# Performance work log

Measured on AMD Instinct MI355X. Metric: run time of the kernel, lower is better.

## Reference

```python
import math
import jax, jax.numpy as jnp
import numpy as np

BLOCK_K = 128  # key/value block size; S_k % BLOCK_K == 0 so no padding/mask needed


def setup_inputs() -> dict:
    key = jax.random.key(0)
    kq, kk, kv = jax.random.split(key, 3)
    B, S, H, Hkv, D = 1, 4096, 16, 8, 128
    return {
        "query": jax.random.normal(kq, (B, S, H, D), dtype=jnp.float32),
        "key": jax.random.normal(kk, (B, S, Hkv, D), dtype=jnp.float32),
        "value": jax.random.normal(kv, (B, S, Hkv, D), dtype=jnp.float32),
    }


def _ring_attention(query, key, value, block_k=BLOCK_K):
    # query: [B, Sq, H, D]; key/value: [B, Sk, Hkv, D]
    scale = 1.0 / math.sqrt(query.shape[-1])
    reps = query.shape[2] // key.shape[2]
    if reps > 1:  # GQA: repeat kv heads to match query heads
        key = jnp.repeat(key, reps, axis=2)
        value = jnp.repeat(value, reps, axis=2)
    q = jnp.transpose(query, (0, 2, 1, 3))   # [B, H, Sq, D]
    k = jnp.transpose(key, (0, 2, 1, 3))     # [B, H, Sk, D]
    v = jnp.transpose(value, (0, 2, 1, 3))
    B, H, Sq, D = q.shape
    Sk = k.shape[2]
    nk = Sk // block_k
    # split keys/values into blocks, block axis leading for scan
    kb = k.reshape(B, H, nk, block_k, D).transpose(2, 0, 1, 3, 4)
    vb = v.reshape(B, H, nk, block_k, D).transpose(2, 0, 1, 3, 4)
    m0 = jnp.full((B, H, Sq), -jnp.inf, dtype=jnp.float32)
    l0 = jnp.zeros((B, H, Sq), dtype=jnp.float32)
    o0 = jnp.zeros((B, H, Sq, D), dtype=jnp.float32)

    def step(carry, kv_blk):
        m, l, o = carry
        k_blk, v_blk = kv_blk
        scores = jnp.einsum('bhqd,bhkd->bhqk', q, k_blk) * scale
        m_new = jnp.maximum(m, jnp.max(scores, axis=-1))
        alpha = jnp.exp(m - m_new)                     # rescale factor (0 on first step)
        p = jnp.exp(scores - m_new[..., None])
        l = l * alpha + jnp.sum(p, axis=-1)
        o = o * alpha[..., None] + jnp.einsum('bhqk,bhkd->bhqd', p, v_blk)
        return (m_new, l, o), None

    (m, l, o), _ = jax.lax.scan(step, (m0, l0, o0), (kb, vb))
    out = o / l[..., None]
    return jnp.transpose(out, (0, 2, 1, 3))  # [B, Sq, H, D]


def reference(query, key, value):
    return _ring_attention(query, key, value)
```

## Files before the change

kernel.cpp:

```cpp
#include <hip/hip_runtime.h>
#include <math.h>


namespace {
constexpr int NH  = 16;
constexpr int NKV = 8;
constexpr int DH  = 128;
constexpr int SK  = 4096;
constexpr int TQ  = 128;
constexpr int NT  = 256;

constexpr int BKM   = 32;
constexpr int NKTM  = SK / BKM;
constexpr int TILEM = BKM * DH;
constexpr size_t WS_NEED = (size_t)2 * NKV * NKTM * TILEM * sizeof(_Float16);

constexpr int BK  = 64;
constexpr int NKT = SK / BK;

typedef _Float16 half8 __attribute__((ext_vector_type(8)));
typedef _Float16 half4 __attribute__((ext_vector_type(4)));
typedef _Float16 half2v __attribute__((ext_vector_type(2)));
typedef __fp16   fp16x2 __attribute__((ext_vector_type(2)));
typedef float  floatx4 __attribute__((ext_vector_type(4)));

#define MFMA16(a, b, c) __builtin_amdgcn_mfma_f32_16x16x32_f16((a), (b), (c), 0, 0, 0)

__global__ __launch_bounds__(256)
void prepack_kv(const float* __restrict__ Kg, const float* __restrict__ Vg,
                _Float16* __restrict__ Kx, _Float16* __restrict__ Vx) {
  __shared__ __align__(16) _Float16 Kb[BKM * 128];
  __shared__ __align__(16) _Float16 Vb[BKM * 130];
  const int id = blockIdx.x;
  const int hk = id & 7;
  const int kt = id >> 3;
  const int t  = threadIdx.x;

#pragma unroll
  for (int it = 0; it < 4; ++it) {
    const int r  = it * 8 + (t >> 5);
    const int c4 = t & 31;
    const size_t src = (((size_t)(kt * BKM + r) * NKV + hk) * DH) + c4 * 4;
    const float4 kf = *reinterpret_cast<const float4*>(Kg + src);
    const float4 vf = *reinterpret_cast<const float4*>(Vg + src);
    half4 kh;
    kh[0] = (_Float16)kf.x; kh[1] = (_Float16)kf.y;
    kh[2] = (_Float16)kf.z; kh[3] = (_Float16)kf.w;
    *reinterpret_cast<half4*>(&Kb[r * 128 + c4 * 4]) = kh;
    half2v v0, v1;
    v0[0] = (_Float16)vf.x; v0[1] = (_Float16)vf.y;
    v1[0] = (_Float16)vf.z; v1[1] = (_Float16)vf.w;
    *reinterpret_cast<half2v*>(&Vb[r * 130 + c4 * 4])     = v0;
    *reinterpret_cast<half2v*>(&Vb[r * 130 + c4 * 4 + 2]) = v1;
  }
  __syncthreads();

  {
    _Float16* out = Kx + (size_t)(hk * NKTM + kt) * TILEM;
#pragma unroll
    for (int it = 0; it < 2; ++it) {
      const int L  = it * 2048 + t * 8;
      const int r  = L >> 7;
      const int gp = (L >> 3) & 15;
      const int c8 = gp ^ (r & 7);
      *reinterpret_cast<half8*>(out + L) =
          *reinterpret_cast<const half8*>(&Kb[r * 128 + c8 * 8]);
    }
  }
  {
    _Float16* out = Vx + (size_t)(hk * NKTM + kt) * TILEM;
#pragma unroll
    for (int it = 0; it < 2; ++it) {
      const int L   = it * 2048 + t * 8;
      const int d   = L >> 5;
      const int kp  = (L >> 3) & 3;
      const int k8  = kp ^ ((d >> 1) & 3);
      half8 hv;
#pragma unroll
      for (int e = 0; e < 8; ++e) hv[e] = Vb[(k8 * 8 + e) * 130 + d];
      *reinterpret_cast<half8*>(out + L) = hv;
    }
  }
}

__global__ __launch_bounds__(NT, 2)
void flash_fwd_pk(const float* __restrict__ Qg,
                  const _Float16* __restrict__ Kx,
                  const _Float16* __restrict__ Vx,
                  float* __restrict__ Og) {
  __shared__ __align__(16) _Float16 KsB[2][TILEM];
  __shared__ __align__(16) _Float16 VtB[2][TILEM];
  __shared__ __align__(16) _Float16 Ps[TQ * 32];

  const int tid  = threadIdx.x;
  const int wave = tid >> 6;
  const int lane = tid & 63;
  const int m16  = lane & 15;
  const int quad = lane >> 4;
  const int hsw  = m16 & 7;
  const int sw2  = (m16 >> 1) & 3;

  const int id = blockIdx.x;
  const int hk = id & 7;
  const int h  = (hk << 1) | ((id >> 3) & 1);
  const int qt = id >> 4;
  const int qr0 = qt * TQ + wave * 32;

  const float4* Q4 = reinterpret_cast<const float4*>(Qg);
  const float scale2 = (float)(0.08838834764831845 * 1.4426950408889634);

  half8 qa[2][4];
#pragma unroll
  for (int mt = 0; mt < 2; ++mt) {
#pragma unroll
    for (int kc = 0; kc < 4; ++kc) {
      const int r = qr0 + mt * 16 + m16;
      const int b = (r * NH + h) * (DH / 4) + kc * 8 + quad * 2;
      float4 x = Q4[b], y = Q4[b + 1];
      half8 f;
      f[0] = (_Float16)(x.x * scale2); f[1] = (_Float16)(x.y * scale2);
      f[2] = (_Float16)(x.z * scale2); f[3] = (_Float16)(x.w * scale2);
      f[4] = (_Float16)(y.x * scale2); f[5] = (_Float16)(y.y * scale2);
      f[6] = (_Float16)(y.z * scale2); f[7] = (_Float16)(y.w * scale2);
      qa[mt][kc] = f;
    }
  }

  floatx4 o[2][8];
#pragma unroll
  for (int mt = 0; mt < 2; ++mt)
#pragma unroll
    for (int nt = 0; nt < 8; ++nt) o[mt][nt] = (floatx4){0.f, 0.f, 0.f, 0.f};
  float lsum[2] = {0.f, 0.f};

  const _Float16* gK = Kx + (size_t)hk * NKTM * TILEM;
  const _Float16* gV = Vx + (size_t)hk * NKTM * TILEM;
  const int soff = tid * 8;

  half8 kr[2], vr[2];
#pragma unroll
  for (int i = 0; i < 2; ++i) {
    kr[i] = *reinterpret_cast<const half8*>(gK + i * 2048 + soff);
    vr[i] = *reinterpret_cast<const half8*>(gV + i * 2048 + soff);
  }

  for (int kt = 0; kt < NKTM; ++kt) {
    const int b = kt & 1;
#pragma unroll
    for (int i = 0; i < 2; ++i) {
      *reinterpret_cast<half8*>(&KsB[b][i * 2048 + soff]) = kr[i];
      *reinterpret_cast<half8*>(&VtB[b][i * 2048 + soff]) = vr[i];
    }
    {
      const int ktn = (kt + 1 < NKTM) ? kt + 1 : kt;
      const _Float16* gKt = gK + (size_t)ktn * TILEM;
      const _Float16* gVt = gV + (size_t)ktn * TILEM;
#pragma unroll
      for (int i = 0; i < 2; ++i) {
        kr[i] = *reinterpret_cast<const half8*>(gKt + i * 2048 + soff);
        vr[i] = *reinterpret_cast<const half8*>(gVt + i * 2048 + soff);
      }
    }
    __syncthreads();

    const _Float16* Ks = KsB[b];
    const _Float16* Vt = VtB[b];

    floatx4 s[2][2];
#pragma unroll
    for (int mt = 0; mt < 2; ++mt)
#pragma unroll
      for (int nt = 0; nt < 2; ++nt) s[mt][nt] = (floatx4){0.f, 0.f, 0.f, 0.f};
#pragma unroll
    for (int nt = 0; nt < 2; ++nt) {
#pragma unroll
      for (int kc = 0; kc < 4; ++kc) {
        const int g = (kc * 4 + quad) ^ hsw;
        half8 kb = *reinterpret_cast<const half8*>(
            &Ks[(nt * 16 + m16) * 128 + g * 8]);
        s[0][nt] = MFMA16(kb, qa[0][kc], s[0][nt]);
        s[1][nt] = MFMA16(kb, qa[1][kc], s[1][nt]);
      }
    }

#pragma unroll
    for (int mt = 0; mt < 2; ++mt) {
      const int prow = wave * 32 + mt * 16 + m16;
#pragma unroll
      for (int nt = 0; nt < 2; ++nt) {
        const float p0 = exp2f(s[mt][nt][0]);
        const float p1 = exp2f(s[mt][nt][1]);
        const float p2 = exp2f(s[mt][nt][2]);
        const float p3 = exp2f(s[mt][nt][3]);
        lsum[mt] += (p0 + p1) + (p2 + p3);
        half4 hv;
        hv[0] = (_Float16)p0; hv[1] = (_Float16)p1;
        hv[2] = (_Float16)p2; hv[3] = (_Float16)p3;
        const int gp = (nt * 2 + (quad >> 1)) ^ sw2;
        *reinterpret_cast<half4*>(&Ps[prow * 32 + gp * 8 + (quad & 1) * 4]) = hv;
      }
    }

    const int gq = quad ^ sw2;
    half8 pa[2];
#pragma unroll
    for (int mt = 0; mt < 2; ++mt)
      pa[mt] = *reinterpret_cast<const half8*>(
          &Ps[(wave * 32 + mt * 16 + m16) * 32 + gq * 8]);
#pragma unroll
    for (int nt = 0; nt < 8; ++nt) {
      half8 vb = *reinterpret_cast<const half8*>(
          &Vt[(nt * 16 + m16) * 32 + gq * 8]);
      o[0][nt] = MFMA16(pa[0], vb, o[0][nt]);
      o[1][nt] = MFMA16(pa[1], vb, o[1][nt]);
    }
  }

#pragma unroll
  for (int mt = 0; mt < 2; ++mt) {
    float ls = lsum[mt];
    ls += __shfl_xor(ls, 16);
    ls += __shfl_xor(ls, 32);
#pragma unroll
    for (int r = 0; r < 4; ++r) {
      const int rq = quad * 4 + r;
      const float inv = 1.f / __shfl(ls, rq);
      const int row = qr0 + mt * 16 + rq;
      const int ob = (row * NH + h) * DH + m16;
#pragma unroll
      for (int nt = 0; nt < 8; ++nt)
        Og[ob + nt * 16] = o[mt][nt][r] * inv;
    }
  }
}

constexpr int KP = 136, VP = 72, PP = 72;

__global__ __launch_bounds__(NT, 2)
void flash_fwd_fb(const float* __restrict__ Qg, const float* __restrict__ Kg,
                  const float* __restrict__ Vg, float* __restrict__ Og) {
  __shared__ _Float16 Ks[BK * KP];
  __shared__ _Float16 Vt[DH * VP];
  __shared__ _Float16 Ps[4 * 32 * PP];

  const int tid  = threadIdx.x;
  const int wave = tid >> 6;
  const int lane = tid & 63;
  const int m16  = lane & 15;
  const int quad = lane >> 4;

  const int id = blockIdx.x;
  const int hk = id & 7;
  const int h  = (hk << 1) | ((id >> 3) & 1);
  const int qt = id >> 4;
  const int qr0 = qt * TQ + wave * 32;

  const float4* Q4 = reinterpret_cast<const float4*>(Qg);
  const float4* K4 = reinterpret_cast<const float4*>(Kg);
  const float scale2 = (float)(0.08838834764831845 * 1.4426950408889634);

  half8 qa[2][4];
#pragma unroll
  for (int mt = 0; mt < 2; ++mt) {
#pragma unroll
    for (int kc = 0; kc < 4; ++kc) {
      const int r = qr0 + mt * 16 + m16;
      const int b = (r * NH + h) * (DH / 4) + kc * 8 + quad * 2;
      float4 x = Q4[b], y = Q4[b + 1];
      half8 f;
      f[0] = (_Float16)(x.x * scale2); f[1] = (_Float16)(x.y * scale2);
      f[2] = (_Float16)(x.z * scale2); f[3] = (_Float16)(x.w * scale2);
      f[4] = (_Float16)(y.x * scale2); f[5] = (_Float16)(y.y * scale2);
      f[6] = (_Float16)(y.z * scale2); f[7] = (_Float16)(y.w * scale2);
      qa[mt][kc] = f;
    }
  }

  floatx4 o[2][8];
#pragma unroll
  for (int mt = 0; mt < 2; ++mt)
#pragma unroll
    for (int nt = 0; nt < 8; ++nt) o[mt][nt] = (floatx4){0.f, 0.f, 0.f, 0.f};
  float lrow[2][4];
#pragma unroll
  for (int mt = 0; mt < 2; ++mt)
#pragma unroll
    for (int r = 0; r < 4; ++r) lrow[mt][r] = 0.f;

  const int kkey = tid >> 2, kdq = tid & 3;
  const int vdim = tid & 127, vkg = tid >> 7;

  float4 kpre[8];
  float  vpre[32];
  {
    const int kb = (kkey * NKV + hk) * (DH / 4);
#pragma unroll
    for (int j = 0; j < 8; ++j) kpre[j] = K4[kb + j * 4 + kdq];
    const int vb = (vkg * 32) * NKV * DH + hk * DH + vdim;
#pragma unroll
    for (int e = 0; e < 32; ++e) vpre[e] = Vg[vb + e * (NKV * DH)];
  }

  for (int kt = 0; kt < NKT; ++kt) {
    __syncthreads();
#pragma unroll
    for (int j = 0; j < 8; ++j) {
      fp16x2 a = __builtin_amdgcn_cvt_pkrtz(kpre[j].x, kpre[j].y);
      fp16x2 b = __builtin_amdgcn_cvt_pkrtz(kpre[j].z, kpre[j].w);
      half4 hv;
      hv[0] = (_Float16)a[0]; hv[1] = (_Float16)a[1];
      hv[2] = (_Float16)b[0]; hv[3] = (_Float16)b[1];
      *reinterpret_cast<half4*>(&Ks[kkey * KP + (j * 4 + kdq) * 4]) = hv;
    }
#pragma unroll
    for (int jj = 0; jj < 4; ++jj) {
      half8 hv;
#pragma unroll
      for (int e = 0; e < 4; ++e) {
        fp16x2 p = __builtin_amdgcn_cvt_pkrtz(vpre[jj * 8 + 2 * e],
                                              vpre[jj * 8 + 2 * e + 1]);
        hv[2 * e] = (_Float16)p[0]; hv[2 * e + 1] = (_Float16)p[1];
      }
      *reinterpret_cast<half8*>(&Vt[vdim * VP + vkg * 32 + jj * 8]) = hv;
    }
    __syncthreads();

    floatx4 s[2][4];
#pragma unroll
    for (int mt = 0; mt < 2; ++mt)
#pragma unroll
      for (int nt = 0; nt < 4; ++nt) s[mt][nt] = (floatx4){0.f, 0.f, 0.f, 0.f};
#pragma unroll
    for (int nt = 0; nt < 4; ++nt) {
#pragma unroll
      for (int kc = 0; kc < 4; ++kc) {
        half8 kb = *reinterpret_cast<const half8*>(
            &Ks[(nt * 16 + m16) * KP + kc * 32 + quad * 8]);
        s[0][nt] = MFMA16(qa[0][kc], kb, s[0][nt]);
        s[1][nt] = MFMA16(qa[1][kc], kb, s[1][nt]);
      }
    }

    {
      const int ktn = (kt + 1 < NKT) ? kt + 1 : kt;
      const int kb = ((ktn * BK + kkey) * NKV + hk) * (DH / 4);
#pragma unroll
      for (int j = 0; j < 8; ++j) kpre[j] = K4[kb + j * 4 + kdq];
      const int vb = (ktn * BK + vkg * 32) * NKV * DH + hk * DH + vdim;
#pragma unroll
      for (int e = 0; e < 32; ++e) vpre[e] = Vg[vb + e * (NKV * DH)];
    }

#pragma unroll
    for (int mt = 0; mt < 2; ++mt) {
#pragma unroll
      for (int nt = 0; nt < 4; ++nt) {
#pragma unroll
        for (int r = 0; r < 4; ++r) {
          const float p = exp2f(s[mt][nt][r]);
          s[mt][nt][r] = p;
          lrow[mt][r] += p;
        }
      }
#pragma unroll
      for (int r = 0; r < 4; ++r) {
        const int prow = (wave * 32 + mt * 16 + quad * 4 + r) * PP;
#pragma unroll
        for (int nt = 0; nt < 4; ++nt)
          Ps[prow + nt * 16 + m16] = (_Float16)s[mt][nt][r];
      }
    }

    half8 pa[2][2];
#pragma unroll
    for (int mt = 0; mt < 2; ++mt)
#pragma unroll
      for (int kc = 0; kc < 2; ++kc)
        pa[mt][kc] = *reinterpret_cast<const half8*>(
            &Ps[(wave * 32 + mt * 16 + m16) * PP + kc * 32 + quad * 8]);
#pragma unroll
    for (int nt = 0; nt < 8; ++nt) {
#pragma unroll
      for (int kc = 0; kc < 2; ++kc) {
        half8 vb = *reinterpret_cast<const half8*>(
            &Vt[(nt * 16 + m16) * VP + kc * 32 + quad * 8]);
        o[0][nt] = MFMA16(pa[0][kc], vb, o[0][nt]);
        o[1][nt] = MFMA16(pa[1][kc], vb, o[1][nt]);
      }
    }
  }

#pragma unroll
  for (int mt = 0; mt < 2; ++mt) {
#pragma unroll
    for (int r = 0; r < 4; ++r) {
      float ls = lrow[mt][r];
      ls += __shfl_xor(ls, 1);
      ls += __shfl_xor(ls, 2);
      ls += __shfl_xor(ls, 4);
      ls += __shfl_xor(ls, 8);
      const float inv = 1.f / ls;
      const int row = qr0 + mt * 16 + quad * 4 + r;
      const int ob = (row * NH + h) * DH + m16;
#pragma unroll
      for (int nt = 0; nt < 8; ++nt)
        Og[ob + nt * 16] = o[mt][nt][r] * inv;
    }
  }
}
}

extern "C" void kernel_launch(void* const* d_in, const int* in_sizes, int n_in,
                              void* d_out, int out_size, void* d_ws, size_t ws_size,
                              hipStream_t stream) {
  const float* Q = (const float*)d_in[0];
  const float* K = (const float*)d_in[1];
  const float* V = (const float*)d_in[2];
  float* O = (float*)d_out;
  if (ws_size >= WS_NEED) {
    _Float16* Kx = (_Float16*)d_ws;
    _Float16* Vx = Kx + (size_t)NKV * NKTM * TILEM;
    prepack_kv<<<1024, 256, 0, stream>>>(K, V, Kx, Vx);
    flash_fwd_pk<<<512, NT, 0, stream>>>(Q, Kx, Vx, O);
  } else {
    flash_fwd_fb<<<512, NT, 0, stream>>>(Q, K, V, O);
  }
}
```

Baseline: 263.0 us.

## Split key range across two blocks per query tile and combine partials

Templates the prepacked flash kernel so each query tile's key sequence is split into two halves handled by separate blocks, doubling the grid. Each half writes unnormalized fp16 partial outputs and fp32 row sums to workspace. A new combine kernel adds the two partials and divides by the summed normalizers. This is meant to raise parallelism and improve load balance across CUs. The cost is an extra launch, extra global traffic for the partials, and possible precision or overflow loss from storing unnormalized outputs in fp16.

```diff
diff --git a/kernel.cpp b/kernel.cpp
--- a/kernel.cpp
+++ b/kernel.cpp
@@ -13,7 +13,10 @@
 constexpr int BKM   = 32;
 constexpr int NKTM  = SK / BKM;
 constexpr int TILEM = BKM * DH;
-constexpr size_t WS_NEED = (size_t)2 * NKV * NKTM * TILEM * sizeof(_Float16);
+constexpr size_t WS_NEED  = (size_t)2 * NKV * NKTM * TILEM * sizeof(_Float16);
+constexpr size_t OP_BYTES = (size_t)2 * SK * NH * DH * sizeof(_Float16);
+constexpr size_t LP_BYTES = (size_t)2 * SK * NH * sizeof(float);
+constexpr size_t WS_SPLIT = WS_NEED + OP_BYTES + LP_BYTES;
 
 constexpr int BK  = 64;
 constexpr int NKT = SK / BK;
@@ -83,11 +86,16 @@
   }
 }
 
+template <bool SPLIT>
 __global__ __launch_bounds__(NT, 2)
 void flash_fwd_pk(const float* __restrict__ Qg,
                   const _Float16* __restrict__ Kx,
                   const _Float16* __restrict__ Vx,
-                  float* __restrict__ Og) {
+                  float* __restrict__ Og,
+                  _Float16* __restrict__ Op,
+                  float* __restrict__ Lp) {
+  constexpr int NTILES = SPLIT ? NKTM / 2 : NKTM;
+
   __shared__ __align__(16) _Float16 KsB[2][TILEM];
   __shared__ __align__(16) _Float16 VtB[2][TILEM];
   __shared__ __align__(16) _Float16 Ps[TQ * 32];
@@ -102,8 +110,10 @@
 
   const int id = blockIdx.x;
   const int hk = id & 7;
-  const int h  = (hk << 1) | ((id >> 3) & 1);
-  const int qt = id >> 4;
+  int sh, hb, qt;
+  if (SPLIT) { sh = (id >> 3) & 1; hb = (id >> 4) & 1; qt = id >> 5; }
+  else       { sh = 0;             hb = (id >> 3) & 1; qt = id >> 4; }
+  const int h   = (hk << 1) | hb;
   const int qr0 = qt * TQ + wave * 32;
 
   const float4* Q4 = reinterpret_cast<const float4*>(Qg);
@@ -133,8 +143,10 @@
     for (int nt = 0; nt < 8; ++nt) o[mt][nt] = (floatx4){0.f, 0.f, 0.f, 0.f};
   float lsum[2] = {0.f, 0.f};
 
-  const _Float16* gK = Kx + (size_t)hk * NKTM * TILEM;
-  const _Float16* gV = Vx + (size_t)hk * NKTM * TILEM;
+  const _Float16* gK =
+      Kx + ((size_t)hk * NKTM + (size_t)sh * NTILES) * TILEM;
+  const _Float16* gV =
+      Vx + ((size_t)hk * NKTM + (size_t)sh * NTILES) * TILEM;
   const int soff = tid * 8;
 
   half8 kr[2], vr[2];
@@ -144,7 +156,7 @@
     vr[i] = *reinterpret_cast<const half8*>(gV + i * 2048 + soff);
   }
 
-  for (int kt = 0; kt < NKTM; ++kt) {
+  for (int kt = 0; kt < NTILES; ++kt) {
     const int b = kt & 1;
 #pragma unroll
     for (int i = 0; i < 2; ++i) {
@@ -152,7 +164,7 @@
       *reinterpret_cast<half8*>(&VtB[b][i * 2048 + soff]) = vr[i];
     }
     {
-      const int ktn = (kt + 1 < NKTM) ? kt + 1 : kt;
+      const int ktn = (kt + 1 < NTILES) ? kt + 1 : kt;
       const _Float16* gKt = gK + (size_t)ktn * TILEM;
       const _Float16* gVt = gV + (size_t)ktn * TILEM;
 #pragma unroll
@@ -216,22 +228,66 @@
     }
   }
 
-#pragma unroll
-  for (int mt = 0; mt < 2; ++mt) {
-    float ls = lsum[mt];
-    ls += __shfl_xor(ls, 16);
-    ls += __shfl_xor(ls, 32);
-#pragma unroll
-    for (int r = 0; r < 4; ++r) {
-      const int rq = quad * 4 + r;
-      const float inv = 1.f / __shfl(ls, rq);
-      const int row = qr0 + mt * 16 + rq;
-      const int ob = (row * NH + h) * DH + m16;
-#pragma unroll
-      for (int nt = 0; nt < 8; ++nt)
-        Og[ob + nt * 16] = o[mt][nt][r] * inv;
-    }
-  }
+  if (!SPLIT) {
+#pragma unroll
+    for (int mt = 0; mt < 2; ++mt) {
+      float ls = lsum[mt];
+      ls += __shfl_xor(ls, 16);
+      ls += __shfl_xor(ls, 32);
+#pragma unroll
+      for (int r = 0; r < 4; ++r) {
+        const int rq = quad * 4 + r;
+        const float inv = 1.f / __shfl(ls, rq);
+        const int row = qr0 + mt * 16 + rq;
+        const int ob = (row * NH + h) * DH + m16;
+#pragma unroll
+        for (int nt = 0; nt < 8; ++nt)
+          Og[ob + nt * 16] = o[mt][nt][r] * inv;
+      }
+    }
+  } else {
+    const size_t opo = (size_t)sh * SK * NH * DH;
+    const int    lpo = sh * SK * NH;
+#pragma unroll
+    for (int mt = 0; mt < 2; ++mt) {
+      float ls = lsum[mt];
+      ls += __shfl_xor(ls, 16);
+      ls += __shfl_xor(ls, 32);
+      if (quad == 0)
+        Lp[lpo + (qr0 + mt * 16 + m16) * NH + h] = ls;
+#pragma unroll
+      for (int r = 0; r < 4; ++r) {
+        const int row = qr0 + mt * 16 + quad * 4 + r;
+        const size_t ob = opo + ((size_t)row * NH + h) * DH + m16;
+#pragma unroll
+        for (int nt = 0; nt < 8; ++nt)
+          Op[ob + nt * 16] = (_Float16)o[mt][nt][r];
+      }
+    }
+  }
+}
+
+__global__ __launch_bounds__(256)
+void combine_o(const _Float16* __restrict__ Op, const float* __restrict__ Lp,
+               float* __restrict__ Og) {
+  constexpr size_t OPH = (size_t)SK * NH * DH;
+  constexpr int    LPH = SK * NH;
+  const int i = blockIdx.x * 256 + threadIdx.x;
+  const half8 a = reinterpret_cast<const half8*>(Op)[i];
+  const half8 b = reinterpret_cast<const half8*>(Op + OPH)[i];
+  const int j = i >> 4;
+  const float inv = 1.f / (Lp[j] + Lp[LPH + j]);
+  float4 r0, r1;
+  r0.x = ((float)a[0] + (float)b[0]) * inv;
+  r0.y = ((float)a[1] + (float)b[1]) * inv;
+  r0.z = ((float)a[2] + (float)b[2]) * inv;
+  r0.w = ((float)a[3] + (float)b[3]) * inv;
+  r1.x = ((float)a[4] + (float)b[4]) * inv;
+  r1.y = ((float)a[5] + (float)b[5]) * inv;
+  r1.z = ((float)a[6] + (float)b[6]) * inv;
+  r1.w = ((float)a[7] + (float)b[7]) * inv;
+  reinterpret_cast<float4*>(Og)[2 * i]     = r0;
+  reinterpret_cast<float4*>(Og)[2 * i + 1] = r1;
 }
 
 constexpr int KP = 136, VP = 72, PP = 72;
@@ -417,11 +473,19 @@
   const float* K = (const float*)d_in[1];
   const float* V = (const float*)d_in[2];
   float* O = (float*)d_out;
-  if (ws_size >= WS_NEED) {
+  if (ws_size >= WS_SPLIT) {
+    _Float16* Kx = (_Float16*)d_ws;
+    _Float16* Vx = Kx + (size_t)NKV * NKTM * TILEM;
+    _Float16* Op = (_Float16*)((char*)d_ws + WS_NEED);
+    float*    Lp = (float*)((char*)d_ws + WS_NEED + OP_BYTES);
+    prepack_kv<<<1024, 256, 0, stream>>>(K, V, Kx, Vx);
+    flash_fwd_pk<true><<<1024, NT, 0, stream>>>(Q, Kx, Vx, nullptr, Op, Lp);
+    combine_o<<<4096, 256, 0, stream>>>(Op, Lp, O);
+  } else if (ws_size >= WS_NEED) {
     _Float16* Kx = (_Float16*)d_ws;
     _Float16* Vx = Kx + (size_t)NKV * NKTM * TILEM;
     prepack_kv<<<1024, 256, 0, stream>>>(K, V, Kx, Vx);
-    flash_fwd_pk<<<512, NT, 0, stream>>>(Q, Kx, Vx, O);
+    flash_fwd_pk<false><<<512, NT, 0, stream>>>(Q, Kx, Vx, O, nullptr, nullptr);
   } else {
     flash_fwd_fb<<<512, NT, 0, stream>>>(Q, K, V, O);
   }
```

New measurement: 280.4 us. 1.07x slower.

## Keep softmax probabilities in registers and permute V prepack to match MFMA layout

Applied to the files above, without the earlier changes.

The score accumulator fragment is fed directly as the A operand of the PV MFMA, so the P tile no longer round-trips through shared memory. For this to be correct, the prepacked V tile is reordered so its key dimension matches the register layout of P. The prepack transpose now reads 32-bit pairs from a repadded shared buffer. The change also switches to the raw exp2 intrinsic and round-toward-zero packed fp16 conversion, which slightly changes rounding.

```diff
diff --git a/kernel.cpp b/kernel.cpp
--- a/kernel.cpp
+++ b/kernel.cpp
@@ -23,6 +23,7 @@
 typedef _Float16 half2v __attribute__((ext_vector_type(2)));
 typedef __fp16   fp16x2 __attribute__((ext_vector_type(2)));
 typedef float  floatx4 __attribute__((ext_vector_type(4)));
+typedef unsigned short ushort8 __attribute__((ext_vector_type(8)));
 
 #define MFMA16(a, b, c) __builtin_amdgcn_mfma_f32_16x16x32_f16((a), (b), (c), 0, 0, 0)
 
@@ -30,7 +31,7 @@
 void prepack_kv(const float* __restrict__ Kg, const float* __restrict__ Vg,
                 _Float16* __restrict__ Kx, _Float16* __restrict__ Vx) {
   __shared__ __align__(16) _Float16 Kb[BKM * 128];
-  __shared__ __align__(16) _Float16 Vb[BKM * 130];
+  __shared__ __align__(16) _Float16 Vb[BKM * 132];
   const int id = blockIdx.x;
   const int hk = id & 7;
   const int kt = id >> 3;
@@ -50,8 +51,8 @@
     half2v v0, v1;
     v0[0] = (_Float16)vf.x; v0[1] = (_Float16)vf.y;
     v1[0] = (_Float16)vf.z; v1[1] = (_Float16)vf.w;
-    *reinterpret_cast<half2v*>(&Vb[r * 130 + c4 * 4])     = v0;
-    *reinterpret_cast<half2v*>(&Vb[r * 130 + c4 * 4 + 2]) = v1;
+    *reinterpret_cast<half2v*>(&Vb[r * 132 + c4 * 4])     = v0;
+    *reinterpret_cast<half2v*>(&Vb[r * 132 + c4 * 4 + 2]) = v1;
   }
   __syncthreads();
 
@@ -69,17 +70,20 @@
   }
   {
     _Float16* out = Vx + (size_t)(hk * NKTM + kt) * TILEM;
-#pragma unroll
-    for (int it = 0; it < 2; ++it) {
-      const int L   = it * 2048 + t * 8;
-      const int d   = L >> 5;
-      const int kp  = (L >> 3) & 3;
-      const int k8  = kp ^ ((d >> 1) & 3);
-      half8 hv;
-#pragma unroll
-      for (int e = 0; e < 8; ++e) hv[e] = Vb[(k8 * 8 + e) * 130 + d];
-      *reinterpret_cast<half8*>(out + L) = hv;
-    }
+    const int dp = t >> 2;
+    const int g  = t & 3;
+    const int ql = g ^ (dp & 3);
+    const int d  = dp * 2;
+    ushort8 lo, hi;
+#pragma unroll
+    for (int j = 0; j < 8; ++j) {
+      const int key = ((j >> 2) * 16) + ql * 4 + (j & 3);
+      const unsigned v = *reinterpret_cast<const unsigned*>(&Vb[key * 132 + d]);
+      lo[j] = (unsigned short)(v & 0xffffu);
+      hi[j] = (unsigned short)(v >> 16);
+    }
+    *reinterpret_cast<ushort8*>(out + d * 32 + g * 8)       = lo;
+    *reinterpret_cast<ushort8*>(out + (d + 1) * 32 + g * 8) = hi;
   }
 }
 
@@ -90,7 +94,6 @@
                   float* __restrict__ Og) {
   __shared__ __align__(16) _Float16 KsB[2][TILEM];
   __shared__ __align__(16) _Float16 VtB[2][TILEM];
-  __shared__ __align__(16) _Float16 Ps[TQ * 32];
 
   const int tid  = threadIdx.x;
   const int wave = tid >> 6;
@@ -178,35 +181,32 @@
         const int g = (kc * 4 + quad) ^ hsw;
         half8 kb = *reinterpret_cast<const half8*>(
             &Ks[(nt * 16 + m16) * 128 + g * 8]);
-        s[0][nt] = MFMA16(kb, qa[0][kc], s[0][nt]);
+        s[0][nt] = MFMA16(kb, qa[0][nt * 0 + kc], s[0][nt]);
         s[1][nt] = MFMA16(kb, qa[1][kc], s[1][nt]);
       }
     }
 
+    union H8 { half8 h; fp16x2 w[4]; };
+    half8 pa[2];
 #pragma unroll
     for (int mt = 0; mt < 2; ++mt) {
-      const int prow = wave * 32 + mt * 16 + m16;
-#pragma unroll
-      for (int nt = 0; nt < 2; ++nt) {
-        const float p0 = exp2f(s[mt][nt][0]);
-        const float p1 = exp2f(s[mt][nt][1]);
-        const float p2 = exp2f(s[mt][nt][2]);
-        const float p3 = exp2f(s[mt][nt][3]);
-        lsum[mt] += (p0 + p1) + (p2 + p3);
-        half4 hv;
-        hv[0] = (_Float16)p0; hv[1] = (_Float16)p1;
-        hv[2] = (_Float16)p2; hv[3] = (_Float16)p3;
-        const int gp = (nt * 2 + (quad >> 1)) ^ sw2;
-        *reinterpret_cast<half4*>(&Ps[prow * 32 + gp * 8 + (quad & 1) * 4]) = hv;
-      }
+      float p[8];
+#pragma unroll
+      for (int nt = 0; nt < 2; ++nt)
+#pragma unroll
+        for (int r = 0; r < 4; ++r)
+          p[nt * 4 + r] = __builtin_amdgcn_exp2f(s[mt][nt][r]);
+      lsum[mt] += ((p[0] + p[1]) + (p[2] + p[3])) +
+                  ((p[4] + p[5]) + (p[6] + p[7]));
+      H8 u;
+      u.w[0] = __builtin_amdgcn_cvt_pkrtz(p[0], p[1]);
+      u.w[1] = __builtin_amdgcn_cvt_pkrtz(p[2], p[3]);
+      u.w[2] = __builtin_amdgcn_cvt_pkrtz(p[4], p[5]);
+      u.w[3] = __builtin_amdgcn_cvt_pkrtz(p[6], p[7]);
+      pa[mt] = u.h;
     }
 
     const int gq = quad ^ sw2;
-    half8 pa[2];
-#pragma unroll
-    for (int mt = 0; mt < 2; ++mt)
-      pa[mt] = *reinterpret_cast<const half8*>(
-          &Ps[(wave * 32 + mt * 16 + m16) * 32 + gq * 8]);
 #pragma unroll
     for (int nt = 0; nt < 8; ++nt) {
       half8 vb = *reinterpret_cast<const half8*>(
```

After: 228.4 us. 1.15x faster.
